# Kernel optimization log

Hardware: AMD Instinct MI355X
Metric: run time of the kernel (lower is better)

## Reference

```python
import jax, jax.numpy as jnp
import numpy as np
from jax import lax

RNN_H = 384      # rnnHiddenSize
HID = 384        # hiddenSize (LSTMCell input size)
POS_EMB = 128    # posEmbSize
POS_NUM = 32
LABELS = 33
BATCH = 16
CHAR_NUM = 1024
ENC = 2 * RNN_H  # 768


def setup_inputs() -> dict:
    key = jax.random.key(0)
    ks = jax.random.split(key, 12)

    def xav(k, shape):
        fan_in = shape[-1]
        return jax.random.normal(k, shape, jnp.float32) / np.sqrt(fan_in)

    return {
        "encoder_output": jax.random.normal(ks[0], (BATCH, CHAR_NUM, ENC), jnp.float32),
        "char_sizes": jax.random.randint(ks[1], (BATCH,), 1, CHAR_NUM, jnp.int32),
        "label_is_sep": jax.random.randint(ks[2], (LABELS,), 0, 2, jnp.int32),
        "label_pos_id": jax.random.randint(ks[3], (LABELS,), 0, POS_NUM, jnp.int32),
        "posEmb": xav(ks[4], (POS_NUM, POS_EMB)),
        "W_ih": xav(ks[5], (4 * RNN_H, HID)),
        "W_hh": xav(ks[6], (4 * RNN_H, RNN_H)),
        "b_ih": jnp.zeros((4 * RNN_H,), jnp.float32),
        "b_hh": jnp.zeros((4 * RNN_H,), jnp.float32),
        "W_lin": xav(ks[7], (LABELS, RNN_H + ENC)),
        "b_lin": jnp.zeros((LABELS,), jnp.float32),
        "W_cmb": xav(ks[8], (HID, ENC + POS_EMB)),
        "b_cmb": jnp.zeros((HID,), jnp.float32),
    }


def reference(encoder_output, char_sizes, label_is_sep, label_pos_id, posEmb,
              W_ih, W_hh, b_ih, b_hh, W_lin, b_lin, W_cmb, b_cmb):
    def lstm_cell(x, h, c):
        g = x @ W_ih.T + b_ih + h @ W_hh.T + b_hh
        i, f, gg, o = jnp.split(g, 4)
        c2 = jax.nn.sigmoid(f) * c + jax.nn.sigmoid(i) * jnp.tanh(gg)
        h2 = jax.nn.sigmoid(o) * jnp.tanh(c2)
        return h2, c2

    def decode(enc, size):  # enc: [T, 2H]; size: scalar int
        T = enc.shape[0]
        # prefix sums make the variable-length avg_pool1d a two-gather op
        prefix = jnp.concatenate([jnp.zeros((1, ENC), enc.dtype),
                                  jnp.cumsum(enc, axis=0)], axis=0)  # [T+1, 2H]

        # initial LSTM step on the (zero) initial last_word_pos_emb
        h, c = lstm_cell(jnp.zeros((HID,), enc.dtype),
                         jnp.zeros((RNN_H,), enc.dtype),
                         jnp.zeros((RNN_H,), enc.dtype))
        zero = jnp.int32(0)
        carry = (h, c, jnp.zeros((POS_EMB,), enc.dtype), zero, zero, zero, zero)

        def step(carry, inp):
            t, enc_t = inp
            h, c, lpe, wlen, nw, npos, plast = carry
            valid = t < size
            out = jnp.tanh(jnp.concatenate([h, enc_t]) @ W_lin.T + b_lin)  # [L]
            aid = jnp.argmax(out)
            is_sep = label_is_sep[aid] > 0
            sep = is_sep & valid
            app = (~is_sep) & valid

            wl_prev = wlen  # length of word that becomes words[-2] on a SEP
            npos_new = jnp.where(sep, npos + 1, npos)
            nw_new = jnp.where(sep, nw + 1, jnp.where(app, jnp.maximum(nw, 1), nw))
            # state.last_pos = pos_id[-2] (the pos before this one), then embed
            lpe_new = jnp.where(sep & (npos_new >= 2), posEmb[plast], lpe)
            plast_new = jnp.where(sep, label_pos_id[aid], plast)
            wlen_new = jnp.where(sep, jnp.int32(1),
                                 jnp.where(app, wlen + 1, wlen))

            # avg_pool1d over previous word chars enc[t-wl_prev : t]
            denom = jnp.maximum(wl_prev, 1).astype(enc.dtype)
            start = jnp.maximum(t - wl_prev, 0)
            avg = (prefix[t] - prefix[start]) / denom  # [2H]
            lwp = jnp.tanh(jnp.concatenate([lpe_new, avg]) @ W_cmb.T + b_cmb)
            h2, c2 = lstm_cell(lwp, h, c)
            do_lstm = sep & (nw_new >= 2)
            h_new = jnp.where(do_lstm, h2, h)
            c_new = jnp.where(do_lstm, c2, c)

            out = jnp.where(valid, out, jnp.zeros_like(out))  # bucket rows
            return (h_new, c_new, lpe_new, wlen_new, nw_new, npos_new, plast_new), out

        _, outs = lax.scan(step, carry, (jnp.arange(T, dtype=jnp.int32), enc))
        return outs  # [T, L]

    outs = jax.vmap(decode)(encoder_output, char_sizes)  # [B, T, L]
    B, T, L = outs.shape
    return jax.nn.log_softmax(outs.reshape(B * T, L), axis=-1)
```

## Files before the change

kernel.cpp:

```cpp
#include <hip/hip_runtime.h>
#include <math.h>


namespace {
constexpr int NB = 16;
constexpr int NT = 1024;
constexpr int NE = 768;
constexpr int NH = 384;
constexpr int NL = 33;
constexpr int ROUNDS = 1024;
constexpr int NSLICE = 16;
constexpr int JS = 24;
constexpr int RS = 96;

constexpr size_t OFF_SL   = 0;
constexpr size_t N_SL     = (size_t)NSLICE * NE * RS;
constexpr size_t OFF_PEW  = OFF_SL + N_SL;
constexpr size_t N_PEW    = 32 * NH;
constexpr size_t OFF_ENCW = OFF_PEW + N_PEW;
constexpr size_t N_ENCW   = (size_t)NB * NT * NL;
constexpr size_t OFF_BS   = OFF_ENCW + N_ENCW;
constexpr size_t OFF_PC   = OFF_BS + 2048;
constexpr size_t N_PC     = (size_t)NB * 1025 * NH;
constexpr size_t OFF_STATE = OFF_PC + N_PC;
constexpr size_t ST_STRIDE = 4096;
constexpr int SX_HWBP = 64;
constexpr int SX_H    = 1280;
constexpr int SX_C    = 2432;
constexpr int IX_T = 0, IX_WLEN = 1, IX_NW = 2, IX_NPOS = 3, IX_PLAST = 4,
              IX_LPEP = 5, IX_LPEE = 6, IX_DONE = 7;
}

__device__ __forceinline__ float sigmf(float x) { return 1.0f / (1.0f + expf(-x)); }

__global__ void k_prep(const float* __restrict__ W_ih, const float* __restrict__ W_hh,
                       const float* __restrict__ W_cmb, const float* __restrict__ posEmb,
                       float* __restrict__ ws) {
    float* SL = ws + OFF_SL;
    float* pw = ws + OFF_PEW;
    const int n1 = (int)N_SL, n2 = (int)N_PEW;
    for (int i = blockIdx.x * blockDim.x + threadIdx.x; i < n1 + n2;
         i += gridDim.x * blockDim.x) {
        if (i < n1) {
            int sl = i / (NE * RS), rem = i % (NE * RS);
            int k = rem / RS, rho = rem % RS;
            int gate = rho / JS, jj = rho % JS;
            int grow = gate * NH + sl * JS + jj;
            SL[i] = (k < NH) ? W_ih[(size_t)grow * NH + k]
                             : W_hh[(size_t)grow * NH + (k - NH)];
        } else {
            int j3 = i - n1;
            int p = j3 / NH, j = j3 % NH;
            const float* pe = posEmb + p * 128;
            const float* wr = W_cmb + (size_t)j * 896;
            float a = 0.f;
            #pragma unroll 4
            for (int k = 0; k < 128; ++k) a += pe[k] * wr[k];
            pw[j3] = a;
        }
    }
}

__global__ void k_encw(const float* __restrict__ enc, const float* __restrict__ W_lin,
                       float* __restrict__ ws) {
    float* encW = ws + OFF_ENCW;
    int gid = blockIdx.x * 256 + threadIdx.x;
    if (gid >= NB * NT * NL) return;
    int bt = gid / NL, l = gid % NL;
    const float4* e4 = (const float4*)(enc + (size_t)bt * NE);
    const float4* w4 = (const float4*)(W_lin + (size_t)l * 1152 + NH);
    float a0 = 0, a1 = 0, a2 = 0, a3 = 0;
    for (int k = 0; k < NE / 4; ++k) {
        float4 e = e4[k], w = w4[k];
        a0 += e.x * w.x; a1 += e.y * w.y; a2 += e.z * w.z; a3 += e.w * w.w;
    }
    encW[gid] = (a0 + a1) + (a2 + a3);
}

__global__ void k_encCmb(const float* __restrict__ enc, const float* __restrict__ W_cmb,
                         float* __restrict__ ws) {
    __shared__ float tile[16][NE];
    float* pc = ws + OFF_PC;
    int blk = blockIdx.x;
    int b = blk >> 6;
    int t0 = (blk & 63) * 16;
    for (int i = threadIdx.x; i < 16 * NE; i += 384) {
        int row = i / NE, k = i % NE;
        tile[row][k] = enc[((size_t)(b * NT + t0 + row)) * NE + k];
    }
    __syncthreads();
    int j = threadIdx.x;
    const float4* w4 = (const float4*)(W_cmb + (size_t)j * 896 + 128);
    float acc[16];
    #pragma unroll
    for (int r = 0; r < 16; ++r) acc[r] = 0.f;
    for (int q = 0; q < NE / 4; ++q) {
        float4 w = w4[q];
        #pragma unroll
        for (int r = 0; r < 16; ++r) {
            acc[r] += w.x * tile[r][q * 4] + w.y * tile[r][q * 4 + 1]
                    + w.z * tile[r][q * 4 + 2] + w.w * tile[r][q * 4 + 3];
        }
    }
    #pragma unroll
    for (int r = 0; r < 16; ++r)
        pc[((size_t)b * 1025 + t0 + r) * NH + j] = acc[r];
}

__global__ void k_prefix(float* __restrict__ ws) {
    float* pc = ws + OFF_PC;
    int id = blockIdx.x * 256 + threadIdx.x;
    if (id >= NB * NH) return;
    int b = id / NH, j = id % NH;
    float* p = pc + ((size_t)b * 1025) * NH + j;
    float s = 0.f;
    for (int t = 0; t < NT; ++t) {
        float x = p[(size_t)t * NH];
        p[(size_t)t * NH] = s;
        s += x;
    }
    p[(size_t)NT * NH] = s;
}

__global__ void k_init(const float* __restrict__ b_ih, const float* __restrict__ b_hh,
                       const float* __restrict__ W_lin, const float* __restrict__ b_lin,
                       float* __restrict__ ws) {
    __shared__ float shh[NH], shc[NH], shw[NL];
    int tid = threadIdx.x;
    if (tid < NH) {
        float gi = b_ih[tid] + b_hh[tid];
        float gg = b_ih[2 * NH + tid] + b_hh[2 * NH + tid];
        float go = b_ih[3 * NH + tid] + b_hh[3 * NH + tid];
        float c = sigmf(gi) * tanhf(gg);
        float h = sigmf(go) * tanhf(c);
        shh[tid] = h; shc[tid] = c;
    }
    __syncthreads();
    if (tid < NL) {
        float a = b_lin[tid];
        for (int k = 0; k < NH; ++k) a += W_lin[(size_t)tid * 1152 + k] * shh[k];
        shw[tid] = a;
    }
    for (int i = tid; i < 4 * NH; i += 1024) ws[OFF_BS + i] = b_ih[i] + b_hh[i];
    __syncthreads();
    for (int s = 0; s < NB; ++s) {
        float* stf = ws + OFF_STATE + (size_t)s * ST_STRIDE;
        int* ii = (int*)stf;
        if (tid < 16) ii[tid] = (tid == IX_LPEP || tid == IX_LPEE) ? -1 : 0;
        if (tid >= 32 && tid < 32 + 576) {
            int i2 = tid - 32, r = i2 / 36, l = i2 % 36;
            stf[SX_HWBP + i2] = (r == 0 && l < NL) ? (shw[l] - b_lin[l]) : 0.f;
        }
        if (tid < NH) { stf[SX_H + tid] = shh[tid]; stf[SX_C + tid] = shc[tid]; }
    }
}

__global__ void k_fill(float* __restrict__ out) {
    int i = blockIdx.x * 256 + threadIdx.x;
    if (i < NB * NT * NL) out[i] = 0.f;
}

__global__ __launch_bounds__(384) void k_round(
    const int* __restrict__ char_sizes,
    const int* __restrict__ label_is_sep, const int* __restrict__ label_pos_id,
    const float* __restrict__ W_lin, const float* __restrict__ b_lin,
    const float* __restrict__ b_cmb, float* __restrict__ ws,
    float* __restrict__ out, const int slot) {

    const int bid = blockIdx.x;
    const int s = bid >> 4;
    const int rh = bid & 15;
    const int tid = threadIdx.x;
    const int lane = tid & 63;
    const int wave = tid >> 6;

    float* stf = ws + OFF_STATE + (size_t)s * ST_STRIDE;
    int* ir = (int*)stf + slot * 16;
    int* iw = (int*)stf + (slot ^ 1) * 16;
    if (ir[IX_DONE]) return;

    const float* hWbp_r = stf + SX_HWBP + slot * 576;
    float*       hWbp_w = stf + SX_HWBP + (slot ^ 1) * 576;
    const float* h_r    = stf + SX_H + slot * 512;
    float*       h_w    = stf + SX_H + (slot ^ 1) * 512;
    float*       cst    = stf + SX_C;

    const float* SLw  = ws + OFF_SL + (size_t)rh * (NE * RS);
    const float* pew  = ws + OFF_PEW;
    const float* encW = ws + OFF_ENCW;
    const float* bsum = ws + OFF_BS;
    const float* pcb  = ws + OFF_PC + (size_t)s * 1025 * NH;

    __shared__ float sh_hWb[40], sh_h[NH], sh_x[NE], sh_part[384], sh_g[RS], sh_h2[JS];
    __shared__ int sh_issep[NL], sh_posid[NL];

    if (tid < NL) {
        float a = b_lin[tid];
        #pragma unroll
        for (int i = 0; i < 16; ++i) a += hWbp_r[i * 36 + tid];
        sh_hWb[tid] = a;
        sh_issep[tid] = label_is_sep[tid];
        sh_posid[tid] = label_pos_id[tid];
    }
    sh_h[tid % NH] = h_r[tid % NH];
    float creg = (tid < JS) ? cst[rh * JS + tid] : 0.f;
    __syncthreads();

    int t = ir[IX_T], wlen = ir[IX_WLEN], nw = ir[IX_NW], npos = ir[IX_NPOS],
        plast = ir[IX_PLAST], lpe_pend = ir[IX_LPEP], lpe_eff = ir[IX_LPEE];
    int size = char_sizes[s]; if (size > NT) size = NT;
    const float* eWb = encW + (size_t)s * NT * NL;
    float* outb = out + (size_t)s * NT * NL;
    int evt_t = -1, evt_start = 0; float evt_den = 1.f;

    for (; t < size; ++t) {
        float ot = (lane < NL) ? tanhf(eWb[(size_t)t * NL + lane] + sh_hWb[lane]) : -INFINITY;
        float bv = ot; int bi = lane;
        #pragma unroll
        for (int d = 32; d; d >>= 1) {
            float ov = __shfl_xor(bv, d);
            int   oi = __shfl_xor(bi, d);
            if (ov > bv || (ov == bv && oi < bi)) { bv = ov; bi = oi; }
        }
        const int aid = bi;
        if (rh == 0 && wave == 0 && lane < NL) outb[(size_t)t * NL + lane] = ot;
        const int issep = sh_issep[aid];
        const int wl_prev = wlen;
        int nw_new;
        if (issep) { npos += 1; nw_new = nw + 1; }
        else       { nw_new = (nw < 1) ? 1 : nw; }
        const int do_l = issep && (nw_new >= 2);
        if (issep && npos >= 2) lpe_pend = plast;
        if (issep) plast = sh_posid[aid];
        wlen = issep ? 1 : wlen + 1;
        nw = nw_new;
        if (do_l) {
            evt_t = t;
            evt_start = (t - wl_prev < 0) ? 0 : (t - wl_prev);
            evt_den = (float)((wl_prev < 1) ? 1 : wl_prev);
            if (lpe_pend >= 0) { lpe_eff = lpe_pend; lpe_pend = -1; }
            ++t;
            break;
        }
    }

    if (evt_t < 0) {
        if (rh == 0 && tid == 0) { iw[IX_DONE] = 1; ir[IX_DONE] = 1; }
        return;
    }

    {
        const int j = tid;
        float avg = (pcb[(size_t)evt_t * NH + j] - pcb[(size_t)evt_start * NH + j]) / evt_den;
        float pv = (lpe_eff >= 0) ? pew[lpe_eff * NH + j] : 0.f;
        sh_x[j]      = tanhf(pv + avg + b_cmb[j]);
        sh_x[NH + j] = sh_h[j];
    }
    __syncthreads();

    {
        const int rho = tid % RS, kq = tid / RS;
        const float* wp = SLw + (size_t)(kq * 192) * RS + rho;
        const float* xp = sh_x + kq * 192;
        float a0 = 0.f, a1 = 0.f, a2 = 0.f, a3 = 0.f;
        #pragma unroll 8
        for (int k = 0; k < 192; k += 4) {
            a0 += wp[(size_t)(k + 0) * RS] * xp[k + 0];
            a1 += wp[(size_t)(k + 1) * RS] * xp[k + 1];
            a2 += wp[(size_t)(k + 2) * RS] * xp[k + 2];
            a3 += wp[(size_t)(k + 3) * RS] * xp[k + 3];
        }
        sh_part[tid] = (a0 + a1) + (a2 + a3);
    }
    __syncthreads();
    if (tid < RS) {
        const int gate = tid / JS, jj = tid % JS;
        const int grow = gate * NH + rh * JS + jj;
        sh_g[tid] = ((sh_part[tid] + sh_part[RS + tid])
                   + (sh_part[2 * RS + tid] + sh_part[3 * RS + tid])) + bsum[grow];
    }
    __syncthreads();
    if (tid < JS) {
        float gi = sh_g[tid], gf = sh_g[JS + tid], gg = sh_g[2 * JS + tid], go = sh_g[3 * JS + tid];
        float c2 = sigmf(gf) * creg + sigmf(gi) * tanhf(gg);
        float h2 = sigmf(go) * tanhf(c2);
        cst[rh * JS + tid] = c2;
        h_w[rh * JS + tid] = h2;
        sh_h2[tid] = h2;
    }
    __syncthreads();
    if (tid < NL) {
        const float* wr = W_lin + (size_t)tid * 1152 + rh * JS;
        float a = 0.f;
        #pragma unroll
        for (int k = 0; k < JS; ++k) a += wr[k] * sh_h2[k];
        hWbp_w[rh * 36 + tid] = a;
    }
    if (rh == 0 && tid == 0) {
        iw[IX_T] = t; iw[IX_WLEN] = wlen; iw[IX_NW] = nw; iw[IX_NPOS] = npos;
        iw[IX_PLAST] = plast; iw[IX_LPEP] = lpe_pend; iw[IX_LPEE] = lpe_eff;
        iw[IX_DONE] = 0;
    }
}

__global__ void k_post(float* __restrict__ out) {
    int row = blockIdx.x * 4 + (threadIdx.x >> 6);
    int lane = threadIdx.x & 63;
    if (row >= NB * NT) return;
    float* p = out + (size_t)row * NL;
    float x = (lane < NL) ? p[lane] : -INFINITY;
    float m = x;
    #pragma unroll
    for (int d = 32; d; d >>= 1) m = fmaxf(m, __shfl_xor(m, d));
    float e = (lane < NL) ? expf(x - m) : 0.f;
    float su = e;
    #pragma unroll
    for (int d = 32; d; d >>= 1) su += __shfl_xor(su, d);
    if (lane < NL) p[lane] = (x - m) - logf(su);
}

extern "C" void kernel_launch(void* const* d_in, const int* in_sizes, int n_in,
                              void* d_out, int out_size, void* d_ws, size_t ws_size,
                              hipStream_t stream) {
    const float* enc          = (const float*)d_in[0];
    const int*   char_sizes   = (const int*)d_in[1];
    const int*   label_is_sep = (const int*)d_in[2];
    const int*   label_pos_id = (const int*)d_in[3];
    const float* posEmb       = (const float*)d_in[4];
    const float* W_ih         = (const float*)d_in[5];
    const float* W_hh         = (const float*)d_in[6];
    const float* b_ih         = (const float*)d_in[7];
    const float* b_hh         = (const float*)d_in[8];
    const float* W_lin        = (const float*)d_in[9];
    const float* b_lin        = (const float*)d_in[10];
    const float* W_cmb        = (const float*)d_in[11];
    const float* b_cmb        = (const float*)d_in[12];
    float* out = (float*)d_out;
    float* ws  = (float*)d_ws;

    hipLaunchKernelGGL(k_prep, dim3(1024), dim3(256), 0, stream,
                       W_ih, W_hh, W_cmb, posEmb, ws);
    hipLaunchKernelGGL(k_encw, dim3((NB * NT * NL + 255) / 256), dim3(256), 0, stream,
                       enc, W_lin, ws);
    hipLaunchKernelGGL(k_encCmb, dim3(1024), dim3(384), 0, stream, enc, W_cmb, ws);
    hipLaunchKernelGGL(k_prefix, dim3((NB * NH + 255) / 256), dim3(256), 0, stream, ws);
    hipLaunchKernelGGL(k_init, dim3(1), dim3(1024), 0, stream,
                       b_ih, b_hh, W_lin, b_lin, ws);
    hipLaunchKernelGGL(k_fill, dim3((NB * NT * NL + 255) / 256), dim3(256), 0, stream, out);

    for (int r = 0; r < ROUNDS; ++r) {
        hipLaunchKernelGGL(k_round, dim3(256), dim3(384), 0, stream,
                           char_sizes, label_is_sep, label_pos_id,
                           W_lin, b_lin, b_cmb, ws, out, r & 1);
    }

    hipLaunchKernelGGL(k_post, dim3((NB * NT + 3) / 4), dim3(256), 0, stream, out);
}
```

Measured before the change: 7.389 ms.

## Overlap recurrent h·W_hh matvec with serial label scan using wave specialization

Only wave 0 now runs the serial argmax/label scan, while other waves compute the h-part of the gate matvec (h·W_hh slice) at the same time, since that part does not depend on the scan outcome. Scan results are passed through shared memory. Afterwards only the x-part (384 inputs) remains on the critical path, split across all 384 threads. This adds shared-memory traffic, and the h-part is wasted work when no event occurs. State writeback moves into wave 0 before the LSTM update.

```diff
diff --git a/kernel.cpp b/kernel.cpp
--- a/kernel.cpp
+++ b/kernel.cpp
@@ -191,80 +191,115 @@
     const float* bsum = ws + OFF_BS;
     const float* pcb  = ws + OFF_PC + (size_t)s * 1025 * NH;
 
-    __shared__ float sh_hWb[40], sh_h[NH], sh_x[NE], sh_part[384], sh_g[RS], sh_h2[JS];
-    __shared__ int sh_issep[NL], sh_posid[NL];
-
-    if (tid < NL) {
-        float a = b_lin[tid];
-        #pragma unroll
-        for (int i = 0; i < 16; ++i) a += hWbp_r[i * 36 + tid];
-        sh_hWb[tid] = a;
-        sh_issep[tid] = label_is_sep[tid];
-        sh_posid[tid] = label_pos_id[tid];
-    }
-    sh_h[tid % NH] = h_r[tid % NH];
+    __shared__ float sh_hWb[40], sh_h[NH], sh_x[NH], sh_part[384], sh_ph[288];
+    __shared__ float sh_g[RS], sh_h2[JS];
+    __shared__ int sh_issep[NL], sh_posid[NL], sh_scan[8];
+
+    sh_h[tid] = h_r[tid];
     float creg = (tid < JS) ? cst[rh * JS + tid] : 0.f;
     __syncthreads();
 
-    int t = ir[IX_T], wlen = ir[IX_WLEN], nw = ir[IX_NW], npos = ir[IX_NPOS],
-        plast = ir[IX_PLAST], lpe_pend = ir[IX_LPEP], lpe_eff = ir[IX_LPEE];
-    int size = char_sizes[s]; if (size > NT) size = NT;
-    const float* eWb = encW + (size_t)s * NT * NL;
-    float* outb = out + (size_t)s * NT * NL;
-    int evt_t = -1, evt_start = 0; float evt_den = 1.f;
-
-    for (; t < size; ++t) {
-        float ot = (lane < NL) ? tanhf(eWb[(size_t)t * NL + lane] + sh_hWb[lane]) : -INFINITY;
-        float bv = ot; int bi = lane;
-        #pragma unroll
-        for (int d = 32; d; d >>= 1) {
-            float ov = __shfl_xor(bv, d);
-            int   oi = __shfl_xor(bi, d);
-            if (ov > bv || (ov == bv && oi < bi)) { bv = ov; bi = oi; }
-        }
-        const int aid = bi;
-        if (rh == 0 && wave == 0 && lane < NL) outb[(size_t)t * NL + lane] = ot;
-        const int issep = sh_issep[aid];
-        const int wl_prev = wlen;
-        int nw_new;
-        if (issep) { npos += 1; nw_new = nw + 1; }
-        else       { nw_new = (nw < 1) ? 1 : nw; }
-        const int do_l = issep && (nw_new >= 2);
-        if (issep && npos >= 2) lpe_pend = plast;
-        if (issep) plast = sh_posid[aid];
-        wlen = issep ? 1 : wlen + 1;
-        nw = nw_new;
-        if (do_l) {
-            evt_t = t;
-            evt_start = (t - wl_prev < 0) ? 0 : (t - wl_prev);
-            evt_den = (float)((wl_prev < 1) ? 1 : wl_prev);
-            if (lpe_pend >= 0) { lpe_eff = lpe_pend; lpe_pend = -1; }
-            ++t;
-            break;
-        }
-    }
-
-    if (evt_t < 0) {
-        if (rh == 0 && tid == 0) { iw[IX_DONE] = 1; ir[IX_DONE] = 1; }
-        return;
-    }
+    if (wave == 0) {
+        if (lane < NL) {
+            sh_issep[lane] = label_is_sep[lane];
+            sh_posid[lane] = label_pos_id[lane];
+            float a = b_lin[lane];
+            #pragma unroll
+            for (int i = 0; i < 16; ++i) a += hWbp_r[i * 36 + lane];
+            sh_hWb[lane] = a;
+        }
+        asm volatile("" ::: "memory");
+
+        int t = ir[IX_T], wlen = ir[IX_WLEN], nw = ir[IX_NW], npos = ir[IX_NPOS],
+            plast = ir[IX_PLAST], lpe_pend = ir[IX_LPEP], lpe_eff = ir[IX_LPEE];
+        int size = char_sizes[s]; if (size > NT) size = NT;
+        const float* eWb = encW + (size_t)s * NT * NL;
+        float* outb = out + (size_t)s * NT * NL;
+        int evt_t = -1, evt_start = 0; float evt_den = 1.f;
+
+        for (; t < size; ++t) {
+            float ot = (lane < NL) ? tanhf(eWb[(size_t)t * NL + lane] + sh_hWb[lane]) : -INFINITY;
+            float bv = ot; int bi = lane;
+            #pragma unroll
+            for (int d = 32; d; d >>= 1) {
+                float ov = __shfl_xor(bv, d);
+                int   oi = __shfl_xor(bi, d);
+                if (ov > bv || (ov == bv && oi < bi)) { bv = ov; bi = oi; }
+            }
+            const int aid = bi;
+            if (rh == 0 && lane < NL) outb[(size_t)t * NL + lane] = ot;
+            const int issep = sh_issep[aid];
+            const int wl_prev = wlen;
+            int nw_new;
+            if (issep) { npos += 1; nw_new = nw + 1; }
+            else       { nw_new = (nw < 1) ? 1 : nw; }
+            const int do_l = issep && (nw_new >= 2);
+            if (issep && npos >= 2) lpe_pend = plast;
+            if (issep) plast = sh_posid[aid];
+            wlen = issep ? 1 : wlen + 1;
+            nw = nw_new;
+            if (do_l) {
+                evt_t = t;
+                evt_start = (t - wl_prev < 0) ? 0 : (t - wl_prev);
+                evt_den = (float)((wl_prev < 1) ? 1 : wl_prev);
+                if (lpe_pend >= 0) { lpe_eff = lpe_pend; lpe_pend = -1; }
+                ++t;
+                break;
+            }
+        }
+
+        if (lane == 0) {
+            sh_scan[0] = evt_t; sh_scan[1] = evt_start;
+            sh_scan[2] = __float_as_int(evt_den); sh_scan[3] = lpe_eff;
+            if (rh == 0) {
+                if (evt_t < 0) {
+                    iw[IX_DONE] = 1; ir[IX_DONE] = 1;
+                } else {
+                    iw[IX_T] = t; iw[IX_WLEN] = wlen; iw[IX_NW] = nw;
+                    iw[IX_NPOS] = npos; iw[IX_PLAST] = plast;
+                    iw[IX_LPEP] = lpe_pend; iw[IX_LPEE] = lpe_eff;
+                    iw[IX_DONE] = 0;
+                }
+            }
+        }
+    } else if (tid >= 64 && tid < 352) {
+        const int u = tid - 64;
+        const int ci = u / 96, rho = u - ci * 96;
+        const float* wp = SLw + (size_t)(NH + ci * 128) * RS + rho;
+        const float* xp = sh_h + ci * 128;
+        float a0 = 0.f, a1 = 0.f, a2 = 0.f, a3 = 0.f;
+        #pragma unroll 8
+        for (int k = 0; k < 128; k += 4) {
+            a0 += wp[(size_t)(k + 0) * RS] * xp[k + 0];
+            a1 += wp[(size_t)(k + 1) * RS] * xp[k + 1];
+            a2 += wp[(size_t)(k + 2) * RS] * xp[k + 2];
+            a3 += wp[(size_t)(k + 3) * RS] * xp[k + 3];
+        }
+        sh_ph[ci * 96 + rho] = (a0 + a1) + (a2 + a3);
+    }
+    __syncthreads();
+
+    const int evt_t = sh_scan[0];
+    if (evt_t < 0) return;
+    const int evt_start = sh_scan[1];
+    const float evt_den = __int_as_float(sh_scan[2]);
+    const int lpe_eff = sh_scan[3];
 
     {
         const int j = tid;
         float avg = (pcb[(size_t)evt_t * NH + j] - pcb[(size_t)evt_start * NH + j]) / evt_den;
         float pv = (lpe_eff >= 0) ? pew[lpe_eff * NH + j] : 0.f;
-        sh_x[j]      = tanhf(pv + avg + b_cmb[j]);
-        sh_x[NH + j] = sh_h[j];
+        sh_x[j] = tanhf(pv + avg + b_cmb[j]);
     }
     __syncthreads();
 
     {
-        const int rho = tid % RS, kq = tid / RS;
-        const float* wp = SLw + (size_t)(kq * 192) * RS + rho;
-        const float* xp = sh_x + kq * 192;
+        const int kq = tid / 96, rho = tid - kq * 96;
+        const float* wp = SLw + (size_t)(kq * 96) * RS + rho;
+        const float* xp = sh_x + kq * 96;
         float a0 = 0.f, a1 = 0.f, a2 = 0.f, a3 = 0.f;
         #pragma unroll 8
-        for (int k = 0; k < 192; k += 4) {
+        for (int k = 0; k < 96; k += 4) {
             a0 += wp[(size_t)(k + 0) * RS] * xp[k + 0];
             a1 += wp[(size_t)(k + 1) * RS] * xp[k + 1];
             a2 += wp[(size_t)(k + 2) * RS] * xp[k + 2];
@@ -273,15 +308,19 @@
         sh_part[tid] = (a0 + a1) + (a2 + a3);
     }
     __syncthreads();
+
     if (tid < RS) {
         const int gate = tid / JS, jj = tid % JS;
         const int grow = gate * NH + rh * JS + jj;
-        sh_g[tid] = ((sh_part[tid] + sh_part[RS + tid])
-                   + (sh_part[2 * RS + tid] + sh_part[3 * RS + tid])) + bsum[grow];
+        sh_g[tid] = (((sh_part[tid] + sh_part[96 + tid])
+                    + (sh_part[192 + tid] + sh_part[288 + tid]))
+                   + ((sh_ph[tid] + sh_ph[96 + tid]) + sh_ph[192 + tid]))
+                  + bsum[grow];
     }
     __syncthreads();
     if (tid < JS) {
-        float gi = sh_g[tid], gf = sh_g[JS + tid], gg = sh_g[2 * JS + tid], go = sh_g[3 * JS + tid];
+        float gi = sh_g[tid], gf = sh_g[JS + tid];
+        float gg = sh_g[2 * JS + tid], go = sh_g[3 * JS + tid];
         float c2 = sigmf(gf) * creg + sigmf(gi) * tanhf(gg);
         float h2 = sigmf(go) * tanhf(c2);
         cst[rh * JS + tid] = c2;
@@ -295,11 +334,6 @@
         #pragma unroll
         for (int k = 0; k < JS; ++k) a += wr[k] * sh_h2[k];
         hWbp_w[rh * 36 + tid] = a;
-    }
-    if (rh == 0 && tid == 0) {
-        iw[IX_T] = t; iw[IX_WLEN] = wlen; iw[IX_NW] = nw; iw[IX_NPOS] = npos;
-        iw[IX_PLAST] = plast; iw[IX_LPEP] = lpe_pend; iw[IX_LPEE] = lpe_eff;
-        iw[IX_DONE] = 0;
     }
 }
 
```

New measurement: 6.904 ms. 6.6% less time.
